# Kernel tuning notes

Hardware: AMD Instinct MI355X
Metric: run time of the kernel (lower is better)

## Reference

```python
import jax, jax.numpy as jnp
import numpy as np

B, L, D, T, V, H = 32, 48, 768, 32, 30522, 768

def build_iou_mask_map():
    # Faithful to the __init__ construction: banded validity mask [32, 33].
    m = np.zeros((32, 33), dtype=np.float32)
    for i in range(0, 32, 1):
        m[i, i + 1:min(i + 17, 33)] = 1.0
    for i in range(0, 32 - 16, 2):
        m[i, list(range(18 + i, 33, 2))] = 1.0
    return jnp.asarray(m)

def setup_inputs() -> dict:
    key = jax.random.key(0)
    ks = jax.random.split(key, 6)
    s = 0.02  # xavier-ish init scale
    return {
        'hidden_states_text': jax.random.normal(ks[0], (B, L, D), jnp.float32),
        'hidden_states_object': jax.random.normal(ks[1], (B, T + 1, D), jnp.float32),
        'w_t1': jax.random.normal(ks[2], (D, H), jnp.float32) * s,
        'b_t1': jnp.zeros((H,), jnp.float32),
        'w_t2': jax.random.normal(ks[3], (H, V), jnp.float32) * s,
        'b_t2': jnp.zeros((V,), jnp.float32),
        'w_i1': jax.random.normal(ks[4], (3 * D, H), jnp.float32) * s,
        'b_i1': jnp.zeros((H,), jnp.float32),
        'w_i2': jax.random.normal(ks[5], (H, 3), jnp.float32) * s,
        'b_i2': jnp.zeros((3,), jnp.float32),
    }

def reference(hidden_states_text, hidden_states_object,
              w_t1, b_t1, w_t2, b_t2, w_i1, b_i1, w_i2, b_i2):
    # final_mlp: Dropout(eval: id) -> Linear -> ReLU -> Dropout -> Linear
    logits_text = jax.nn.relu(hidden_states_text @ w_t1 + b_t1) @ w_t2 + b_t2  # [B,L,V]

    hc = hidden_states_object                # [B, T+1, D]
    t = hc.shape[1] - 1
    s_idx = jnp.arange(t)                    # [T]
    e_idx = jnp.arange(t + 1)                # [T+1]
    # (0.5*(s+e)).long() == floor division for non-negative ints
    c_idx = (s_idx[:, None] + e_idx[None, :]) // 2          # [T, T+1]
    c_point = hc[:, c_idx, :]                                # [B, T, T+1, D] gather
    d = hc.shape[-1]
    s_pts = jnp.broadcast_to(hc[:, :-1, None, :], (hc.shape[0], t, t + 1, d))
    e_pts = jnp.broadcast_to(hc[:, None, :, :], (hc.shape[0], t, t + 1, d))
    sce = jnp.concatenate([s_pts, c_point, e_pts], axis=-1)  # [B, T, T+1, 3D]

    # final_mlp_3: Linear(3D->H) -> ReLU -> Dropout(id) -> Linear(H->3)
    h = jax.nn.relu(jnp.einsum('bstf,fh->bsth', sce, w_i1) + b_i1)
    logits_iou = jnp.einsum('bsth,hk->bstk', h, w_i2) + b_i2  # [B,T,T+1,3]
    logits_iou = jnp.transpose(logits_iou, (0, 3, 1, 2))      # [B,3,T,T+1]

    return logits_text, logits_iou, build_iou_mask_map()
```

## Files before the change

kernel.cpp:

```cpp
#include <hip/hip_runtime.h>

typedef unsigned short u16;
typedef short v8s __attribute__((ext_vector_type(8)));
typedef float v4f __attribute__((ext_vector_type(4)));

#define KDIM 768
#define M_TEXT 1536
#define N_VOCAB 30522
#define N_VOCAB_PAD 30592
#define M_HC 1056
#define M_HC_PAD 1152
#define N_IOU 2304
#define OUT_IOU_OFF 46881792
#define OUT_MASK_OFF 46983168

__device__ __forceinline__ u16 f2bf(float f) {
  unsigned u = __float_as_uint(f);
  u += 0x7fffu + ((u >> 16) & 1u);
  return (u16)(u >> 16);
}

__global__ __launch_bounds__(256) void prep_cvt(const float* __restrict__ xt_in,
                                                const float* __restrict__ hc_in,
                                                u16* __restrict__ xt,
                                                u16* __restrict__ hcb) {
  const int NXT = M_TEXT * KDIM / 4;
  int i = blockIdx.x * 256 + threadIdx.x;
  if (i < NXT) {
    float4 v = ((const float4*)xt_in)[i];
    ushort4 o; o.x = f2bf(v.x); o.y = f2bf(v.y); o.z = f2bf(v.z); o.w = f2bf(v.w);
    ((ushort4*)xt)[i] = o;
  } else {
    int j = i - NXT;
    int row = j / 192;
    float4 v = make_float4(0.f, 0.f, 0.f, 0.f);
    if (row < M_HC) v = ((const float4*)hc_in)[j];
    ushort4 o; o.x = f2bf(v.x); o.y = f2bf(v.y); o.z = f2bf(v.z); o.w = f2bf(v.w);
    ((ushort4*)hcb)[j] = o;
  }
}

__global__ __launch_bounds__(256) void transpose_cvt(const float* __restrict__ in,
                                                     u16* __restrict__ out,
                                                     int C, long inBatch, long outBatch) {
  __shared__ float tile[64][65];
  const float* ip = in + (long)blockIdx.z * inBatch;
  u16* op = out + (long)blockIdx.z * outBatch;
  int r0 = blockIdx.x * 64, c0 = blockIdx.y * 64;
  int tx = threadIdx.x & 63, tg = threadIdx.x >> 6;
#pragma unroll
  for (int i = 0; i < 16; ++i) {
    int r = tg + i * 4;
    int gc = c0 + tx;
    tile[r][tx] = (gc < C) ? ip[(long)(r0 + r) * C + gc] : 0.f;
  }
  __syncthreads();
#pragma unroll
  for (int i = 0; i < 16; ++i) {
    int cc = tg + i * 4;
    op[(long)(c0 + cc) * KDIM + r0 + tx] = f2bf(tile[tx][cc]);
  }
}

__global__ void mask_kernel(float* __restrict__ out) {
  int idx = blockIdx.x * 256 + threadIdx.x;
  if (idx >= 1056) return;
  int i = idx / 33, j = idx % 33;
  float v = 0.f;
  int hi = min(i + 17, 33);
  if (j >= i + 1 && j < hi) v = 1.f;
  if ((i & 1) == 0 && i < 16 && j >= 18 + i && ((j - (18 + i)) & 1) == 0) v = 1.f;
  out[OUT_MASK_OFF + idx] = v;
}

template <int MODE>
__global__ __launch_bounds__(256)
void gemm_bt(const u16* __restrict__ A, const u16* __restrict__ BT,
             float* __restrict__ fout, u16* __restrict__ bfout,
             const float* __restrict__ bias, int ldc, int nmax) {
  __shared__ u16 sA[128 * 32];
  __shared__ u16 sB[128 * 32];
  const int tid = threadIdx.x;
  const int wid = tid >> 6;
  const int lane = tid & 63;
  const int lrow = lane & 15;
  const int quad = lane >> 4;
  const int wm = (wid & 1) * 64;
  const int wn = (wid >> 1) * 64;
  const int m0 = blockIdx.y * 128;
  const int n0 = blockIdx.x * 128;

  const int srow = wid * 32 + (lane >> 2);
  const int scol = (lane & 3) * 8;
  const u16* gA = A + (long)(m0 + srow) * KDIM + scol;
  const u16* gB = BT + (long)(n0 + srow) * KDIM + scol;
  u16* lA = &sA[(wid * 32) * 32];
  u16* lB = &sB[(wid * 32) * 32];

  v4f acc[4][4];
#pragma unroll
  for (int i = 0; i < 4; ++i)
#pragma unroll
    for (int j = 0; j < 4; ++j) acc[i][j] = (v4f){0.f, 0.f, 0.f, 0.f};

  const v8s* pA = (const v8s*)sA;
  const v8s* pB = (const v8s*)sB;
  const int ia0 = (wm + lrow) * 4 + quad;
  const int ib0 = (wn + lrow) * 4 + quad;

  for (int kt = 0; kt < KDIM / 32; ++kt) {
    const u16* ga = gA + kt * 32;
    const u16* gb = gB + kt * 32;
    __builtin_amdgcn_global_load_lds((const __attribute__((address_space(1))) void*)ga,
                                     (__attribute__((address_space(3))) void*)lA, 16, 0, 0);
    __builtin_amdgcn_global_load_lds((const __attribute__((address_space(1))) void*)(ga + 16 * KDIM),
                                     (__attribute__((address_space(3))) void*)(lA + 16 * 32), 16, 0, 0);
    __builtin_amdgcn_global_load_lds((const __attribute__((address_space(1))) void*)gb,
                                     (__attribute__((address_space(3))) void*)lB, 16, 0, 0);
    __builtin_amdgcn_global_load_lds((const __attribute__((address_space(1))) void*)(gb + 16 * KDIM),
                                     (__attribute__((address_space(3))) void*)(lB + 16 * 32), 16, 0, 0);
    __syncthreads();

    v8s af[4], bfr[4];
#pragma unroll
    for (int mt = 0; mt < 4; ++mt) af[mt] = pA[ia0 + mt * 64];
#pragma unroll
    for (int nt = 0; nt < 4; ++nt) bfr[nt] = pB[ib0 + nt * 64];
#pragma unroll
    for (int mt = 0; mt < 4; ++mt)
#pragma unroll
      for (int nt = 0; nt < 4; ++nt)
        acc[mt][nt] = __builtin_amdgcn_mfma_f32_16x16x32_bf16(af[mt], bfr[nt], acc[mt][nt], 0, 0, 0);
    __syncthreads();
  }

#pragma unroll
  for (int nt = 0; nt < 4; ++nt) {
    int c = n0 + wn + nt * 16 + lrow;
    float bv = 0.f;
    if (MODE == 0) { if (c < nmax) bv = bias[c]; }
    if (MODE == 1) bv = bias[c];
#pragma unroll
    for (int mt = 0; mt < 4; ++mt) {
#pragma unroll
      for (int r = 0; r < 4; ++r) {
        int row = m0 + wm + mt * 16 + quad * 4 + r;
        float v = acc[mt][nt][r] + bv;
        if (MODE == 0) {
          if (c < nmax) fout[(long)row * ldc + c] = v;
        } else if (MODE == 1) {
          bfout[(long)row * ldc + c] = f2bf(fmaxf(v, 0.f));
        } else {
          fout[(long)row * ldc + c] = v;
        }
      }
    }
  }
}

__global__ __launch_bounds__(256) void iou_combine(const float* __restrict__ Xcat,
                                                   const float* __restrict__ b1,
                                                   const float* __restrict__ w2,
                                                   const float* __restrict__ b2,
                                                   float* __restrict__ out) {
  int gw = (blockIdx.x * 256 + threadIdx.x) >> 6;
  int lane = threadIdx.x & 63;
  if (gw >= 32 * 32 * 33) return;
  int b = gw / 1056;
  int rem = gw % 1056;
  int s = rem / 33;
  int t = rem % 33;
  int cidx = (s + t) >> 1;
  const float* ps = Xcat + (long)(b * 33 + s) * N_IOU;
  const float* pc = Xcat + (long)(b * 33 + cidx) * N_IOU + 768;
  const float* pe = Xcat + (long)(b * 33 + t) * N_IOU + 1536;
  float a0 = 0.f, a1 = 0.f, a2 = 0.f;
#pragma unroll
  for (int j = 0; j < 3; ++j) {
    int h0 = j * 256 + lane * 4;
    float4 vs = *(const float4*)(ps + h0);
    float4 vc = *(const float4*)(pc + h0);
    float4 ve = *(const float4*)(pe + h0);
    float4 vb = *(const float4*)(b1 + h0);
    const float* fs = (const float*)&vs;
    const float* fc = (const float*)&vc;
    const float* fe = (const float*)&ve;
    const float* fb = (const float*)&vb;
#pragma unroll
    for (int c = 0; c < 4; ++c) {
      float v = fmaxf(fs[c] + fc[c] + fe[c] + fb[c], 0.f);
      int h = h0 + c;
      a0 += v * w2[h * 3 + 0];
      a1 += v * w2[h * 3 + 1];
      a2 += v * w2[h * 3 + 2];
    }
  }
#pragma unroll
  for (int off = 32; off > 0; off >>= 1) {
    a0 += __shfl_down(a0, off, 64);
    a1 += __shfl_down(a1, off, 64);
    a2 += __shfl_down(a2, off, 64);
  }
  if (lane == 0) {
    int base = OUT_IOU_OFF + b * 3168 + s * 33 + t;
    out[base + 0 * 1056] = a0 + b2[0];
    out[base + 1 * 1056] = a1 + b2[1];
    out[base + 2 * 1056] = a2 + b2[2];
  }
}

extern "C" void kernel_launch(void* const* d_in, const int* in_sizes, int n_in,
                              void* d_out, int out_size, void* d_ws, size_t ws_size,
                              hipStream_t stream) {
  const float* hst  = (const float*)d_in[0];
  const float* hso  = (const float*)d_in[1];
  const float* w_t1 = (const float*)d_in[2];
  const float* b_t1 = (const float*)d_in[3];
  const float* w_t2 = (const float*)d_in[4];
  const float* b_t2 = (const float*)d_in[5];
  const float* w_i1 = (const float*)d_in[6];
  const float* b_i1 = (const float*)d_in[7];
  const float* w_i2 = (const float*)d_in[8];
  const float* b_i2 = (const float*)d_in[9];
  float* out = (float*)d_out;

  char* ws = (char*)d_ws;
  u16*   w_t2T = (u16*)(ws + 0);
  u16*   xt    = (u16*)(ws + 46989312);
  u16*   w_t1T = (u16*)(ws + 49348608);
  u16*   htext = (u16*)(ws + 50528256);
  u16*   hcb   = (u16*)(ws + 52887552);
  u16*   w_i1T = (u16*)(ws + 54657024);
  float* Xcat  = (float*)(ws + 58195968);

  prep_cvt<<<dim3(2016), dim3(256), 0, stream>>>(hst, hso, xt, hcb);
  transpose_cvt<<<dim3(12, 12, 1), dim3(256), 0, stream>>>(w_t1, w_t1T, 768, 0, 0);
  transpose_cvt<<<dim3(12, N_VOCAB_PAD / 64, 1), dim3(256), 0, stream>>>(w_t2, w_t2T, N_VOCAB, 0, 0);
  transpose_cvt<<<dim3(12, 12, 3), dim3(256), 0, stream>>>(w_i1, w_i1T, 768, 768L * 768, 768L * 768);
  mask_kernel<<<dim3(5), dim3(256), 0, stream>>>(out);

  gemm_bt<1><<<dim3(KDIM / 128, M_TEXT / 128), dim3(256), 0, stream>>>(
      xt, w_t1T, nullptr, htext, b_t1, KDIM, KDIM);
  gemm_bt<0><<<dim3(N_VOCAB_PAD / 128, M_TEXT / 128), dim3(256), 0, stream>>>(
      htext, w_t2T, out, nullptr, b_t2, N_VOCAB, N_VOCAB);

  gemm_bt<2><<<dim3(N_IOU / 128, M_HC_PAD / 128), dim3(256), 0, stream>>>(
      hcb, w_i1T, Xcat, nullptr, nullptr, N_IOU, N_IOU);
  iou_combine<<<dim3(8448), dim3(256), 0, stream>>>(Xcat, b_i1, w_i2, b_i2, out);
}
```

Measured before the change: 526.0 us.

## Add 256x256-tile pipelined GEMM with direct-to-LDS loads for vocab projection

Replaces the generic 128x128 bf16 GEMM for the large text-vocab projection with a dedicated 512-thread kernel that computes 256x256 tiles. The kernel loads operands straight into LDS via global_load_lds, uses XOR-swizzled shared layouts, double-buffers A and B with staggered prefetch, raises priority around MFMA bursts, and applies a grid swizzle for L2 locality. The goal is more operand reuse and overlap of memory with MFMA work on the dominant GEMM. The cost is a large hand-scheduled kernel with tight barrier and waitcnt logic. It also relies on clamped edge loads for the padded vocab tail, and its bigger tiles mean fewer blocks in flight.

New measurement: 533.7 us. Within noise of the previous version (+1.5%).

```diff
diff --git a/kernel.cpp b/kernel.cpp
--- a/kernel.cpp
+++ b/kernel.cpp
@@ -138,7 +138,6 @@
   for (int nt = 0; nt < 4; ++nt) {
     int c = n0 + wn + nt * 16 + lrow;
     float bv = 0.f;
-    if (MODE == 0) { if (c < nmax) bv = bias[c]; }
     if (MODE == 1) bv = bias[c];
 #pragma unroll
     for (int mt = 0; mt < 4; ++mt) {
@@ -146,9 +145,7 @@
       for (int r = 0; r < 4; ++r) {
         int row = m0 + wm + mt * 16 + quad * 4 + r;
         float v = acc[mt][nt][r] + bv;
-        if (MODE == 0) {
-          if (c < nmax) fout[(long)row * ldc + c] = v;
-        } else if (MODE == 1) {
+        if (MODE == 1) {
           bfout[(long)row * ldc + c] = f2bf(fmaxf(v, 0.f));
         } else {
           fout[(long)row * ldc + c] = v;
@@ -157,6 +154,203 @@
     }
   }
 }
+
+#define DSREAD_B(sB) do {                                                  \
+    const u16* _b = (sB) + bBase;                                          \
+    _Pragma("unroll")                                                      \
+    for (int _nf = 0; _nf < 4; ++_nf) {                                    \
+      bfr[_nf][0] = *(const v8s*)(_b + _nf * 1024 + c0);                   \
+      bfr[_nf][1] = *(const v8s*)(_b + _nf * 1024 + c1);                   \
+    } } while (0)
+
+#define DSREAD_A(sA, q) do {                                               \
+    const u16* _a = (sA) + aBase + (q) * 2048;                             \
+    af[0][0] = *(const v8s*)(_a + c0);                                     \
+    af[0][1] = *(const v8s*)(_a + c1);                                     \
+    af[1][0] = *(const v8s*)(_a + 1024 + c0);                              \
+    af[1][1] = *(const v8s*)(_a + 1024 + c1);                              \
+  } while (0)
+
+#define MFMA_Q(q) do {                                                     \
+    _Pragma("unroll")                                                      \
+    for (int _m = 0; _m < 2; ++_m)                                         \
+      _Pragma("unroll")                                                    \
+      for (int _nf = 0; _nf < 4; ++_nf) {                                  \
+        acc[2*(q)+_m][_nf] = __builtin_amdgcn_mfma_f32_16x16x32_bf16(      \
+            af[_m][0], bfr[_nf][0], acc[2*(q)+_m][_nf], 0, 0, 0);          \
+        acc[2*(q)+_m][_nf] = __builtin_amdgcn_mfma_f32_16x16x32_bf16(      \
+            af[_m][1], bfr[_nf][1], acc[2*(q)+_m][_nf], 0, 0, 0);          \
+      } } while (0)
+
+#define BAR_SB() do { __builtin_amdgcn_s_barrier();                        \
+                      __builtin_amdgcn_sched_barrier(0); } while (0)
+#define LGKM0() do { asm volatile("s_waitcnt lgkmcnt(0)" ::: "memory");    \
+                     __builtin_amdgcn_sched_barrier(0); } while (0)
+
+__global__ __launch_bounds__(512, 2)
+void gemm_big(const u16* __restrict__ A, const u16* __restrict__ BT,
+              float* __restrict__ out, const float* __restrict__ bias) {
+  __shared__ u16 sbuf[2][2][256 * 64];
+
+  const int id = blockIdx.x;
+  const int swz = (id & 7) * 90 + (id >> 3);
+  const int mt = swz % 6;
+  const int nt = swz / 6;
+  const int m0 = mt * 256, n0 = nt * 256;
+
+  const int tid = threadIdx.x;
+  const int wid = tid >> 6;
+  const int lane = tid & 63;
+  const int l3 = lane >> 3;
+  const int l7 = lane & 7;
+  const int lrow = lane & 15;
+  const int quad = lane >> 4;
+  const int wr = wid >> 2;
+  const int wc = wid & 3;
+
+  const int xc = (l7 ^ l3) * 8;
+  const u16* Ag = A  + (long)(m0 + wid * 16 + l3) * KDIM + xc;
+  const u16* Bg = BT + (long)(n0 + wid * 16 + l3) * KDIM + xc;
+
+  u16* const sA0 = &sbuf[0][0][0];
+  u16* const sB0 = &sbuf[0][1][0];
+  u16* const sA1 = &sbuf[1][0][0];
+  u16* const sB1 = &sbuf[1][1][0];
+
+  auto stageA = [&](u16* sdst, int kt, int h) {
+#pragma unroll
+    for (int j = 0; j < 2; ++j)
+      __builtin_amdgcn_global_load_lds(
+          (const __attribute__((address_space(1))) void*)(Ag + (long)kt * 64 +
+                                                          (long)((h * 128 + j * 8) * KDIM)),
+          (__attribute__((address_space(3))) void*)(sdst + (h * 128 + wid * 16 + j * 8) * 64),
+          16, 0, 0);
+  };
+  auto stageB = [&](u16* sdst, int kt, int h) {
+    const int hh = (n0 + h * 128 >= N_VOCAB_PAD) ? 0 : h;
+#pragma unroll
+    for (int j = 0; j < 2; ++j)
+      __builtin_amdgcn_global_load_lds(
+          (const __attribute__((address_space(1))) void*)(Bg + (long)kt * 64 +
+                                                          (long)((hh * 128 + j * 8) * KDIM)),
+          (__attribute__((address_space(3))) void*)(sdst + (h * 128 + wid * 16 + j * 8) * 64),
+          16, 0, 0);
+  };
+
+  const int aBase = (wr * 128 + lrow) * 64;
+  const int bBase = (wc * 64 + lrow) * 64;
+  const int xls = (lrow & 7) * 8;
+  const int c0 = (quad * 8) ^ xls;
+  const int c1 = c0 ^ 32;
+
+  v4f acc[8][4];
+#pragma unroll
+  for (int i = 0; i < 8; ++i)
+#pragma unroll
+    for (int j = 0; j < 4; ++j) acc[i][j] = (v4f){0.f, 0.f, 0.f, 0.f};
+
+  v8s bfr[4][2];
+  v8s af[2][2];
+
+  stageA(sA0, 0, 0); stageA(sA0, 0, 1);
+  stageB(sB0, 0, 0); stageB(sB0, 0, 1);
+  stageB(sB1, 1, 0); stageB(sB1, 1, 1);
+  asm volatile("s_waitcnt vmcnt(4)" ::: "memory");
+  __builtin_amdgcn_sched_barrier(0);
+  BAR_SB();
+
+#pragma unroll 1
+  for (int it = 0; it < 6; ++it) {
+    const int kA1 = 2 * it + 1;
+    const int kB0 = 2 * it + 2;
+    const int kB1 = 2 * it + 3;
+    const bool more = (it < 5);
+
+    DSREAD_B(sB0);
+    DSREAD_A(sA0, 0);
+    stageA(sA1, kA1, 0);
+    __builtin_amdgcn_s_barrier();
+    LGKM0();
+    __builtin_amdgcn_s_setprio(1); MFMA_Q(0); __builtin_amdgcn_s_setprio(0);
+    BAR_SB();
+
+    DSREAD_A(sA0, 1);
+    stageA(sA1, kA1, 1);
+    __builtin_amdgcn_s_barrier();
+    LGKM0();
+    __builtin_amdgcn_s_setprio(1); MFMA_Q(1); __builtin_amdgcn_s_setprio(0);
+    BAR_SB();
+
+    DSREAD_A(sA0, 2);
+    if (more) stageB(sB0, kB0, 0);
+    __builtin_amdgcn_s_barrier();
+    LGKM0();
+    __builtin_amdgcn_s_setprio(1); MFMA_Q(2); __builtin_amdgcn_s_setprio(0);
+    BAR_SB();
+
+    DSREAD_A(sA0, 3);
+    if (more) stageB(sB0, kB0, 1);
+    __builtin_amdgcn_s_barrier();
+    LGKM0();
+    __builtin_amdgcn_s_setprio(1); MFMA_Q(3); __builtin_amdgcn_s_setprio(0);
+    if (more) { asm volatile("s_waitcnt vmcnt(4)" ::: "memory"); }
+    else      { asm volatile("s_waitcnt vmcnt(0)" ::: "memory"); }
+    __builtin_amdgcn_sched_barrier(0);
+    BAR_SB();
+
+    DSREAD_B(sB1);
+    DSREAD_A(sA1, 0);
+    if (more) stageA(sA0, kB0, 0);
+    __builtin_amdgcn_s_barrier();
+    LGKM0();
+    __builtin_amdgcn_s_setprio(1); MFMA_Q(0); __builtin_amdgcn_s_setprio(0);
+    BAR_SB();
+
+    DSREAD_A(sA1, 1);
+    if (more) stageA(sA0, kB0, 1);
+    __builtin_amdgcn_s_barrier();
+    LGKM0();
+    __builtin_amdgcn_s_setprio(1); MFMA_Q(1); __builtin_amdgcn_s_setprio(0);
+    BAR_SB();
+
+    DSREAD_A(sA1, 2);
+    if (more) stageB(sB1, kB1, 0);
+    __builtin_amdgcn_s_barrier();
+    LGKM0();
+    __builtin_amdgcn_s_setprio(1); MFMA_Q(2); __builtin_amdgcn_s_setprio(0);
+    BAR_SB();
+
+    DSREAD_A(sA1, 3);
+    if (more) stageB(sB1, kB1, 1);
+    __builtin_amdgcn_s_barrier();
+    LGKM0();
+    __builtin_amdgcn_s_setprio(1); MFMA_Q(3); __builtin_amdgcn_s_setprio(0);
+    if (more) { asm volatile("s_waitcnt vmcnt(4)" ::: "memory");
+                __builtin_amdgcn_sched_barrier(0); }
+    BAR_SB();
+  }
+
+#pragma unroll
+  for (int nf = 0; nf < 4; ++nf) {
+    const int c = n0 + wc * 64 + nf * 16 + lrow;
+    if (c < N_VOCAB) {
+      const float bv = bias[c];
+#pragma unroll
+      for (int mf = 0; mf < 8; ++mf) {
+        const long r0 = m0 + wr * 128 + mf * 16 + quad * 4;
+#pragma unroll
+        for (int rr = 0; rr < 4; ++rr)
+          out[(r0 + rr) * (long)N_VOCAB + c] = acc[mf][nf][rr] + bv;
+      }
+    }
+  }
+}
+
+#undef DSREAD_B
+#undef DSREAD_A
+#undef MFMA_Q
+#undef BAR_SB
+#undef LGKM0
 
 __global__ __launch_bounds__(256) void iou_combine(const float* __restrict__ Xcat,
                                                    const float* __restrict__ b1,
@@ -241,8 +435,7 @@
 
   gemm_bt<1><<<dim3(KDIM / 128, M_TEXT / 128), dim3(256), 0, stream>>>(
       xt, w_t1T, nullptr, htext, b_t1, KDIM, KDIM);
-  gemm_bt<0><<<dim3(N_VOCAB_PAD / 128, M_TEXT / 128), dim3(256), 0, stream>>>(
-      htext, w_t2T, out, nullptr, b_t2, N_VOCAB, N_VOCAB);
+  gemm_big<<<dim3(720), dim3(512), 0, stream>>>(htext, w_t2T, out, b_t2);
 
   gemm_bt<2><<<dim3(N_IOU / 128, M_HC_PAD / 128), dim3(256), 0, stream>>>(
       hcb, w_i1T, Xcat, nullptr, nullptr, N_IOU, N_IOU);
```
